# Kernel tuning notes

Hardware: AMD Instinct MI355X
Metric: run time of the kernel (lower is better)

## Reference

```python
import math
import jax, jax.numpy as jnp
import numpy as np

NUM_HEADS = 12
NUM_LANDMARKS = 32

def iterative_inv(mat, n_iter=6):
    # mat: [B, H, m, m] row-stochastic kernel; Newton-Schulz pseudo-inverse
    m = mat.shape[-1]
    I = jnp.eye(m, dtype=mat.dtype)
    K = mat
    # 'else' branch: per-(B,H) normalization by max column sum
    denom = jnp.max(jnp.sum(K, axis=-2), axis=-1)[..., None, None]
    V = jnp.swapaxes(K, -1, -2) / denom
    for _ in range(n_iter):
        KV = jnp.matmul(K, V)
        V = jnp.matmul(0.25 * V, 13.0 * I - jnp.matmul(KV, 15.0 * I - jnp.matmul(KV, 7.0 * I - KV)))
    return V

def setup_inputs() -> dict:
    key = jax.random.key(0)
    k1, k2, k3 = jax.random.split(key, 3)
    B, N, C = 8, 2048, 768
    x = jax.random.normal(k1, (B, N, C), dtype=jnp.float32)
    w_qkv = jax.random.normal(k2, (C, 3 * C), dtype=jnp.float32) * (1.0 / math.sqrt(C))
    w_proj = jax.random.normal(k3, (C, C), dtype=jnp.float32) * (1.0 / math.sqrt(C))
    b_proj = jnp.zeros((C,), dtype=jnp.float32)
    return {"x": x, "w_qkv": w_qkv, "w_proj": w_proj, "b_proj": b_proj}

def reference(x, w_qkv, w_proj, b_proj):
    B, N, C = x.shape
    H = NUM_HEADS
    d = C // H
    m = NUM_LANDMARKS
    qkv = (x @ w_qkv).reshape(B, N, 3, H, d).transpose(2, 0, 3, 1, 4)  # [3,B,H,N,d]
    Q, K, V = qkv[0], qkv[1], qkv[2]
    scale = 1.0 / math.sqrt(math.sqrt(d))
    Q = Q * scale
    K = K * scale
    # landmark pooling: mean over contiguous chunks of size N//m
    Q_l = Q.reshape(B, H, m, N // m, d).mean(axis=-2)  # [B,H,m,d]
    K_l = K.reshape(B, H, m, N // m, d).mean(axis=-2)
    kernel_1 = jax.nn.softmax(jnp.einsum('bhnd,bhmd->bhnm', Q, K_l), axis=-1)   # [B,H,N,m]
    kernel_2 = jax.nn.softmax(jnp.einsum('bhmd,bhkd->bhmk', Q_l, K_l), axis=-1) # [B,H,m,m]
    kernel_3 = jax.nn.softmax(jnp.einsum('bhmd,bhnd->bhmn', Q_l, K), axis=-1)   # [B,H,m,N]
    X = jnp.matmul(jnp.matmul(kernel_1, iterative_inv(kernel_2)), jnp.matmul(kernel_3, V))  # [B,H,N,d]
    X = X.transpose(0, 2, 1, 3).reshape(B, N, C)
    return X @ w_proj + b_proj
```

## Files before the change

### kernel.cpp

```cpp
#include <hip/hip_runtime.h>
#include <hip/hip_bf16.h>

typedef __hip_bfloat16 bf16;
typedef __attribute__((ext_vector_type(8))) __bf16 bf16x8;
typedef __attribute__((ext_vector_type(4))) float f32x4;

#define NB 8
#define SEQ 2048
#define CH 768
#define NH 12
#define HD 64
#define NL 32
#define BHT (NB*NH)
#define TOK (NB*SEQ)
#define QK_SCALE 0.35355339059327379f

#define BAR() __builtin_amdgcn_s_barrier()
#define WLGKM0() __asm__ __volatile__("s_waitcnt lgkmcnt(0)" ::: "memory")
#define WVM(n) __asm__ __volatile__("s_waitcnt vmcnt(" #n ")" ::: "memory")

__device__ __forceinline__ void async_ld16(const bf16* g, bf16* l) {
    unsigned loff = (unsigned)__builtin_amdgcn_readfirstlane((int)(unsigned)(uintptr_t)l);
    __builtin_amdgcn_global_load_lds(
        (const __attribute__((address_space(1))) unsigned*)(uintptr_t)g,
        (__attribute__((address_space(3))) unsigned*)(uintptr_t)loff, 16, 0, 0);
}

#define PREP_G0 (TOK*CH/2048)
#define PREP_G1 ((3*CH/32)*(CH/32))
#define PREP_G2 ((CH/32)*(CH/32))
__global__ __launch_bounds__(256) void prep(const float* __restrict__ x, bf16* __restrict__ xb,
                                            const float* __restrict__ w_qkv, bf16* __restrict__ wqkvT,
                                            const float* __restrict__ w_proj, bf16* __restrict__ wprojT) {
    __shared__ float tile[32][33];
    const int bid = blockIdx.x;
    const int t = threadIdx.x;
    if (bid < PREP_G0) {
        size_t i = ((size_t)bid * 256 + t) * 8;
        float4 a = *reinterpret_cast<const float4*>(x + i);
        float4 b = *reinterpret_cast<const float4*>(x + i + 4);
        alignas(16) bf16 tmp[8];
        tmp[0] = __float2bfloat16(a.x); tmp[1] = __float2bfloat16(a.y);
        tmp[2] = __float2bfloat16(a.z); tmp[3] = __float2bfloat16(a.w);
        tmp[4] = __float2bfloat16(b.x); tmp[5] = __float2bfloat16(b.y);
        tmp[6] = __float2bfloat16(b.z); tmp[7] = __float2bfloat16(b.w);
        *reinterpret_cast<uint4*>(xb + i) = *reinterpret_cast<const uint4*>(tmp);
        return;
    }
    const float* in; bf16* outp; int Hrows, Wcols, bx, by;
    if (bid < PREP_G0 + PREP_G1) {
        int tb = bid - PREP_G0;
        in = w_qkv; outp = wqkvT; Hrows = CH; Wcols = 3 * CH;
        bx = (tb % (3 * CH / 32)) * 32; by = (tb / (3 * CH / 32)) * 32;
    } else {
        int tb = bid - PREP_G0 - PREP_G1;
        in = w_proj; outp = wprojT; Hrows = CH; Wcols = CH;
        bx = (tb % (CH / 32)) * 32; by = (tb / (CH / 32)) * 32;
    }
    int tx = t & 31, ty = t >> 5;
    for (int i = 0; i < 32; i += 8)
        tile[ty + i][tx] = in[(size_t)(by + ty + i) * Wcols + bx + tx];
    __syncthreads();
    for (int i = 0; i < 32; i += 8)
        outp[(size_t)(bx + ty + i) * Hrows + by + tx] = __float2bfloat16(tile[tx][ty + i]);
}

template <int EPI>
__global__ __launch_bounds__(256, 2) void gemm_bt(
    const bf16* __restrict__ A, const bf16* __restrict__ Bt,
    int Nout, int Kdim,
    bf16* __restrict__ q, bf16* __restrict__ k, bf16* __restrict__ vt,
    float* __restrict__ Ql, float* __restrict__ Kl,
    float* __restrict__ outp, const float* __restrict__ bias_f) {
    __shared__ __align__(16) bf16 As[2][128 * 64];
    __shared__ __align__(16) bf16 Bs[2][192 * 64];
    const int t = threadIdx.x;
    const int wave = t >> 6, lane = t & 63;
    const int quad = lane >> 4, l15 = lane & 15;
    const int wr = wave >> 1, wc = wave & 1;

    int p = blockIdx.y * gridDim.x + blockIdx.x;
    int xcd = p & 7, j = p >> 3;
    int gx = gridDim.x;
    int bn = j % gx;
    int bm = (j / gx) * 8 + xcd;
    const int bm0 = bm * 128;
    const int bn0 = bn * 192;

    const int T = Kdim >> 6;

    const int srow = t >> 3;
    const int scol = (((t & 7) ^ (srow & 7)) << 3);
    const bf16* Abase = A + (size_t)(bm0 + srow) * Kdim + scol;
    const bf16* Bbase = Bt + (size_t)(bn0 + srow) * Kdim + scol;

    auto stA = [&](int kt, int c) {
        async_ld16(Abase + (size_t)(c * 32) * Kdim + kt * 64,
                   &As[kt & 1][c * 2048 + t * 8]);
    };
    auto stB = [&](int kt, int c) {
        async_ld16(Bbase + (size_t)(c * 32) * Kdim + kt * 64,
                   &Bs[kt & 1][c * 2048 + t * 8]);
    };

    const int swk[2] = { (quad ^ (l15 & 7)) << 3, ((4 + quad) ^ (l15 & 7)) << 3 };
    const bf16* arow = &As[0][(wr * 64 + l15) * 64];
    const bf16* brow = &Bs[0][(wc * 96 + l15) * 64];

    f32x4 acc[4][6];
    const f32x4 zero4 = {0.f, 0.f, 0.f, 0.f};
    #pragma unroll
    for (int i = 0; i < 4; i++)
        #pragma unroll
        for (int jj = 0; jj < 6; jj++) acc[i][jj] = zero4;

    stA(0, 0); stA(0, 2); stB(0, 0); stB(0, 1); stB(0, 3); stB(0, 4);
    stB(0, 2); stB(0, 5);
    stA(0, 1); stA(0, 3);
    WVM(4);
    BAR();

    bf16x8 a[4][2], b[6][2];
    for (int kt = 0; kt < T; kt++) {
        const int cur = kt & 1;
        const bool nxt = (kt + 1 < T);
        const bf16* ab = arow + cur * 8192;
        const bf16* bb = brow + cur * 12288;

        #pragma unroll
        for (int mi = 0; mi < 2; mi++)
            #pragma unroll
            for (int kk = 0; kk < 2; kk++)
                a[mi][kk] = *reinterpret_cast<const bf16x8*>(ab + mi * 1024 + swk[kk]);
        #pragma unroll
        for (int ni = 0; ni < 3; ni++)
            #pragma unroll
            for (int kk = 0; kk < 2; kk++)
                b[ni][kk] = *reinterpret_cast<const bf16x8*>(bb + ni * 1024 + swk[kk]);
        if (nxt) { stA(kt + 1, 0); stA(kt + 1, 2); stB(kt + 1, 0); }
        BAR(); WLGKM0();
        __builtin_amdgcn_s_setprio(1);
        #pragma unroll
        for (int mi = 0; mi < 2; mi++)
            #pragma unroll
            for (int ni = 0; ni < 3; ni++)
                #pragma unroll
                for (int kk = 0; kk < 2; kk++)
                    acc[mi][ni] = __builtin_amdgcn_mfma_f32_16x16x32_bf16(a[mi][kk], b[ni][kk], acc[mi][ni], 0, 0, 0);
        __builtin_amdgcn_s_setprio(0);
        if (nxt) { WVM(5); } else { WVM(2); }
        BAR();

        #pragma unroll
        for (int ni = 3; ni < 6; ni++)
            #pragma unroll
            for (int kk = 0; kk < 2; kk++)
                b[ni][kk] = *reinterpret_cast<const bf16x8*>(bb + ni * 1024 + swk[kk]);
        if (nxt) { stB(kt + 1, 1); stB(kt + 1, 3); stB(kt + 1, 4); }
        BAR(); WLGKM0();
        __builtin_amdgcn_s_setprio(1);
        #pragma unroll
        for (int mi = 0; mi < 2; mi++)
            #pragma unroll
            for (int ni = 3; ni < 6; ni++)
                #pragma unroll
                for (int kk = 0; kk < 2; kk++)
                    acc[mi][ni] = __builtin_amdgcn_mfma_f32_16x16x32_bf16(a[mi][kk], b[ni][kk], acc[mi][ni], 0, 0, 0);
        __builtin_amdgcn_s_setprio(0);
        if (nxt) { WVM(6); } else { WVM(0); }
        BAR();

        #pragma unroll
        for (int mi = 2; mi < 4; mi++)
            #pragma unroll
            for (int kk = 0; kk < 2; kk++)
                a[mi][kk] = *reinterpret_cast<const bf16x8*>(ab + mi * 1024 + swk[kk]);
        if (nxt) { stB(kt + 1, 2); stB(kt + 1, 5); stA(kt + 1, 1); stA(kt + 1, 3); }
        BAR(); WLGKM0();
        __builtin_amdgcn_s_setprio(1);
        #pragma unroll
        for (int mi = 2; mi < 4; mi++)
            #pragma unroll
            for (int ni = 0; ni < 6; ni++)
                #pragma unroll
                for (int kk = 0; kk < 2; kk++)
                    acc[mi][ni] = __builtin_amdgcn_mfma_f32_16x16x32_bf16(a[mi][kk], b[ni][kk], acc[mi][ni], 0, 0, 0);
        __builtin_amdgcn_s_setprio(0);
        if (nxt) { WVM(4); }
        BAR();
    }

    if (EPI == 0) {
        const int which = bn0 / CH;
        const int rem0 = bn0 - which * CH + wc * 96;
        const int b = bm0 >> 11;
        const int nnb = (bm0 & 2047) + wr * 64;
        if (which < 2) {
            bf16* dstqk = (which == 0) ? q : k;
            float* dstl = (which == 0) ? Ql : Kl;
            const int la = nnb >> 6;
            #pragma unroll
            for (int ni = 0; ni < 6; ni++) {
                int rem = rem0 + ni * 16;
                int h = rem >> 6;
                int dd = (rem & 63) + l15;
                int bh = b * NH + h;
                float colsum = 0.f;
                #pragma unroll
                for (int mi = 0; mi < 4; mi++) {
                    int nn0 = nnb + mi * 16 + quad * 4;
                    #pragma unroll
                    for (int r = 0; r < 4; r++) {
                        float val = acc[mi][ni][r];
                        colsum += val;
                        dstqk[((size_t)bh * SEQ + nn0 + r) * HD + dd] = __float2bfloat16(val * QK_SCALE);
                    }
                }
                colsum += __shfl_xor(colsum, 16);
                colsum += __shfl_xor(colsum, 32);
                if (quad == 0)
                    dstl[((size_t)bh * NL + la) * HD + dd] = colsum * (QK_SCALE / 64.f);
            }
        } else {
            #pragma unroll
            for (int ni = 0; ni < 6; ni++) {
                int rem = rem0 + ni * 16;
                int h = rem >> 6;
                int dd = (rem & 63) + l15;
                int bh = b * NH + h;
                #pragma unroll
                for (int mi = 0; mi < 4; mi++) {
                    int nn0 = nnb + mi * 16 + quad * 4;
                    alignas(8) bf16 four[4];
                    #pragma unroll
                    for (int r = 0; r < 4; r++) four[r] = __float2bfloat16(acc[mi][ni][r]);
                    *reinterpret_cast<uint2*>(&vt[((size_t)bh * HD + dd) * SEQ + nn0]) =
                        *reinterpret_cast<const uint2*>(four);
                }
            }
        }
    } else {
        #pragma unroll
        for (int ni = 0; ni < 6; ni++) {
            int col = bn0 + wc * 96 + ni * 16 + l15;
            float bb = bias_f[col];
            #pragma unroll
            for (int mi = 0; mi < 4; mi++)
                #pragma unroll
                for (int r = 0; r < 4; r++) {
                    int row = bm0 + wr * 64 + mi * 16 + quad * 4 + r;
                    outp[(size_t)row * Nout + col] = acc[mi][ni][r] + bb;
                }
        }
    }
}

__device__ inline void mm32(float* Cm, const float* Am, const float* Bm, int t) {
    for (int e = t; e < 1024; e += 256) {
        int i = e >> 5, jj = e & 31;
        float s = 0.f;
        #pragma unroll
        for (int kk = 0; kk < 32; kk++) s += Am[i * 32 + kk] * Bm[kk * 32 + jj];
        Cm[e] = s;
    }
}

__global__ __launch_bounds__(256) void k3_pv(const float* __restrict__ Ql,
                                             const float* __restrict__ Klm,
                                             const bf16* __restrict__ Kb,
                                             const bf16* __restrict__ Vt,
                                             float* __restrict__ Opart,
                                             float* __restrict__ Spart,
                                             float* __restrict__ Vinv) {
    __shared__ __align__(16) char smem[69632];
    const int bh = blockIdx.x;
    const int t = threadIdx.x;

    if (blockIdx.y == 0) {
        float* K2 = (float*)smem;
        float* Vv = K2 + 1024;
        float* KV = K2 + 2048;
        float* Ta = K2 + 3072;
        float* Tb = K2 + 4096;
        float* red = K2 + 5120;
        const float* ql = Ql + (size_t)bh * NL * HD;
        const float* kl = Klm + (size_t)bh * NL * HD;

        for (int e = t; e < 1024; e += 256) {
            int i = e >> 5, jj = e & 31;
            float s = 0.f;
            #pragma unroll 8
            for (int d = 0; d < 64; d++) s += ql[i * 64 + d] * kl[jj * 64 + d];
            K2[e] = s;
        }
        __syncthreads();
        if (t < 32) {
            float mx = -1e30f;
            for (int jj = 0; jj < 32; jj++) mx = fmaxf(mx, K2[t * 32 + jj]);
            float sm = 0.f;
            for (int jj = 0; jj < 32; jj++) { float e = __expf(K2[t * 32 + jj] - mx); K2[t * 32 + jj] = e; sm += e; }
            float inv = 1.f / sm;
            for (int jj = 0; jj < 32; jj++) K2[t * 32 + jj] *= inv;
        }
        __syncthreads();
        if (t < 32) {
            float cs = 0.f;
            for (int i = 0; i < 32; i++) cs += K2[i * 32 + t];
            red[t] = cs;
        }
        __syncthreads();
        if (t == 0) {
            float mx = red[0];
            for (int jj = 1; jj < 32; jj++) mx = fmaxf(mx, red[jj]);
            red[32] = mx;
        }
        __syncthreads();
        float invden = 1.f / red[32];
        for (int e = t; e < 1024; e += 256) {
            int i = e >> 5, jj = e & 31;
            Vv[e] = K2[jj * 32 + i] * invden;
        }
        __syncthreads();
        for (int it = 0; it < 6; it++) {
            mm32(KV, K2, Vv, t);
            __syncthreads();
            for (int e = t; e < 1024; e += 256) { int i = e >> 5, jj = e & 31; Ta[e] = ((i == jj) ? 7.f : 0.f) - KV[e]; }
            __syncthreads();
            mm32(Tb, KV, Ta, t);
            __syncthreads();
            for (int e = t; e < 1024; e += 256) { int i = e >> 5, jj = e & 31; Tb[e] = ((i == jj) ? 15.f : 0.f) - Tb[e]; }
            __syncthreads();
            mm32(Ta, KV, Tb, t);
            __syncthreads();
            for (int e = t; e < 1024; e += 256) { int i = e >> 5, jj = e & 31; Ta[e] = ((i == jj) ? 13.f : 0.f) - Ta[e]; }
            __syncthreads();
            mm32(Tb, Vv, Ta, t);
            __syncthreads();
            for (int e = t; e < 1024; e += 256) Vv[e] = 0.25f * Tb[e];
            __syncthreads();
        }
        for (int e = t; e < 1024; e += 256)
            Vinv[(size_t)bh * 1024 + e] = Vv[e];
        return;
    }

    bf16* Pw0 = (bf16*)smem;
    float* Ored0 = (float*)(smem + 34816);
    float* Sred = (float*)(smem + 34816 + 33280);
    const int cc = blockIdx.y - 1;
    const int n0 = cc * 512;
    const int w = t >> 6, lane = t & 63;
    const int quad = lane >> 4, l15 = lane & 15;

    const bf16* Kbh = Kb + (size_t)bh * SEQ * HD;
    const bf16* Vtb = Vt + (size_t)bh * HD * SEQ;

    bf16x8 af[2][2];
    #pragma unroll
    for (int mt = 0; mt < 2; mt++)
        #pragma unroll
        for (int kh = 0; kh < 2; kh++) {
            const float* src = Ql + (size_t)bh * NL * HD + (mt * 16 + l15) * 64 + kh * 32 + quad * 8;
            alignas(16) bf16 tmp[8];
            #pragma unroll
            for (int jj = 0; jj < 8; jj++) tmp[jj] = __float2bfloat16(src[jj]);
            af[mt][kh] = *reinterpret_cast<const bf16x8*>(tmp);
        }

    const f32x4 zero4 = {0.f, 0.f, 0.f, 0.f};
    f32x4 oacc[2][4];
    #pragma unroll
    for (int mt = 0; mt < 2; mt++)
        #pragma unroll
        for (int nd = 0; nd < 4; nd++) oacc[mt][nd] = zero4;
    float rs[2][4];
    #pragma unroll
    for (int mt = 0; mt < 2; mt++)
        #pragma unroll
        for (int r = 0; r < 4; r++) rs[mt][r] = 0.f;

    bf16* Pme = Pw0 + w * (32 * 136);

    #pragma unroll
    for (int h = 0; h < 2; h++) {
        f32x4 sacc[2][4];
        #pragma unroll
        for (int mt = 0; mt < 2; mt++)
            #pragma unroll
            for (int nt = 0; nt < 4; nt++) sacc[mt][nt] = zero4;
        #pragma unroll
        for (int nt = 0; nt < 4; nt++) {
            int n = n0 + w * 128 + h * 64 + nt * 16 + l15;
            bf16x8 kf0 = *reinterpret_cast<const bf16x8*>(&Kbh[(size_t)n * HD + quad * 8]);
            bf16x8 kf1 = *reinterpret_cast<const bf16x8*>(&Kbh[(size_t)n * HD + 32 + quad * 8]);
            #pragma unroll
            for (int mt = 0; mt < 2; mt++) {
                sacc[mt][nt] = __builtin_amdgcn_mfma_f32_16x16x32_bf16(af[mt][0], kf0, sacc[mt][nt], 0, 0, 0);
                sacc[mt][nt] = __builtin_amdgcn_mfma_f32_16x16x32_bf16(af[mt][1], kf1, sacc[mt][nt], 0, 0, 0);
            }
        }
        #pragma unroll
        for (int mt = 0; mt < 2; mt++)
            #pragma unroll
            for (int nt = 0; nt < 4; nt++)
                #pragma unroll
                for (int r = 0; r < 4; r++) {
                    float pv = __expf(sacc[mt][nt][r]);
                    rs[mt][r] += pv;
                    int row = mt * 16 + quad * 4 + r;
                    Pme[row * 136 + h * 64 + nt * 16 + l15] = __float2bfloat16(pv);
                }
    }
    __asm__ __volatile__("s_waitcnt lgkmcnt(0)" ::: "memory");

    #pragma unroll
    for (int kt = 0; kt < 4; kt++) {
        bf16x8 pa[2];
        pa[0] = *reinterpret_cast<const bf16x8*>(&Pme[l15 * 136 + kt * 32 + quad * 8]);
        pa[1] = *reinterpret_cast<const bf16x8*>(&Pme[(16 + l15) * 136 + kt * 32 + quad * 8]);
        int kbase = n0 + w * 128 + kt * 32 + quad * 8;
        #pragma unroll
        for (int nd = 0; nd < 4; nd++) {
            bf16x8 bv = *reinterpret_cast<const bf16x8*>(&Vtb[(size_t)(nd * 16 + l15) * SEQ + kbase]);
            oacc[0][nd] = __builtin_amdgcn_mfma_f32_16x16x32_bf16(pa[0], bv, oacc[0][nd], 0, 0, 0);
            oacc[1][nd] = __builtin_amdgcn_mfma_f32_16x16x32_bf16(pa[1], bv, oacc[1][nd], 0, 0, 0);
        }
    }

    #pragma unroll
    for (int mt = 0; mt < 2; mt++)
        #pragma unroll
        for (int r = 0; r < 4; r++) {
            float v = rs[mt][r];
            #pragma unroll
            for (int o = 1; o < 16; o <<= 1) v += __shfl_xor(v, o);
            rs[mt][r] = v;
        }
    if (l15 == 0)
        #pragma unroll
        for (int mt = 0; mt < 2; mt++)
            #pragma unroll
            for (int r = 0; r < 4; r++)
                Sred[w * 32 + mt * 16 + quad * 4 + r] = rs[mt][r];
    #pragma unroll
    for (int mt = 0; mt < 2; mt++)
        #pragma unroll
        for (int nd = 0; nd < 4; nd++)
            #pragma unroll
            for (int r = 0; r < 4; r++)
                Ored0[w * (32 * 65) + (mt * 16 + quad * 4 + r) * 65 + nd * 16 + l15] = oacc[mt][nd][r];
    __syncthreads();

    float* Op = Opart + ((size_t)bh * 4 + cc) * (NL * HD);
    for (int e = t; e < 2048; e += 256) {
        int m = e >> 6, dd = e & 63;
        Op[e] = Ored0[0 * (32 * 65) + m * 65 + dd] + Ored0[1 * (32 * 65) + m * 65 + dd] +
                Ored0[2 * (32 * 65) + m * 65 + dd] + Ored0[3 * (32 * 65) + m * 65 + dd];
    }
    if (t < 32)
        Spart[((size_t)bh * 4 + cc) * NL + t] = Sred[t] + Sred[32 + t] + Sred[64 + t] + Sred[96 + t];
}

__global__ __launch_bounds__(256) void combine_w2(const float* __restrict__ Opart,
                                                  const float* __restrict__ Spart,
                                                  const float* __restrict__ Vinv,
                                                  float* __restrict__ W2) {
    __shared__ float K3[2048];
    __shared__ float Vv[1024];
    __shared__ float stot[32];
    const int bh = blockIdx.x;
    const int t = threadIdx.x;

    if (t < 32) {
        const float* sp = Spart + (size_t)bh * 4 * NL;
        stot[t] = sp[t] + sp[32 + t] + sp[64 + t] + sp[96 + t];
    }
    {
        const float* op = Opart + (size_t)bh * 4 * (NL * HD);
        for (int e = t; e < 2048; e += 256)
            K3[e] = op[e] + op[2048 + e] + op[4096 + e] + op[6144 + e];
    }
    for (int e = t; e < 1024; e += 256)
        Vv[e] = Vinv[(size_t)bh * 1024 + e];
    __syncthreads();
    for (int e = t; e < 2048; e += 256) K3[e] *= (1.f / stot[e >> 6]);
    __syncthreads();
    for (int e = t; e < 2048; e += 256) {
        int i = e >> 6, dd = e & 63;
        float s = 0.f;
        #pragma unroll
        for (int kk = 0; kk < 32; kk++) s += Vv[i * 32 + kk] * K3[kk * 64 + dd];
        W2[(size_t)bh * NL * HD + e] = s;
    }
}

__global__ __launch_bounds__(256) void rows_fused(const bf16* __restrict__ Qb,
                                                  const float* __restrict__ Kl,
                                                  const float* __restrict__ W2,
                                                  bf16* __restrict__ Xp) {
    __shared__ __align__(16) bf16 Klb[32 * 64];
    __shared__ __align__(16) bf16 W2t[64 * 32];
    __shared__ __align__(16) bf16 Pw[4][32 * 40];
    const int bh = blockIdx.x, tile = blockIdx.y;
    const int t = threadIdx.x, w = t >> 6, lane = t & 63;
    const int quad = lane >> 4, l15 = lane & 15;

    {
        const float* ksrc = Kl + (size_t)bh * NL * HD;
        const float* wsrc = W2 + (size_t)bh * NL * HD;
        int e0 = t * 8;
        #pragma unroll
        for (int jj = 0; jj < 8; jj++) {
            int e = e0 + jj;
            Klb[e] = __float2bfloat16(ksrc[e]);
            int kk = e >> 6, dd = e & 63;
            W2t[dd * 32 + kk] = __float2bfloat16(wsrc[e]);
        }
    }
    __syncthreads();

    const int b = bh / NH, h = bh - b * NH;
    const int row0 = tile * 128 + w * 32;
    const bf16* qbase = Qb + ((size_t)bh * SEQ + row0) * HD;

    const f32x4 zero4 = {0.f, 0.f, 0.f, 0.f};
    f32x4 sacc[2][2];
    #pragma unroll
    for (int mt = 0; mt < 2; mt++)
        #pragma unroll
        for (int nt = 0; nt < 2; nt++) sacc[mt][nt] = zero4;
    #pragma unroll
    for (int kh = 0; kh < 2; kh++) {
        bf16x8 bk0 = *reinterpret_cast<const bf16x8*>(&Klb[(l15) * 64 + kh * 32 + quad * 8]);
        bf16x8 bk1 = *reinterpret_cast<const bf16x8*>(&Klb[(16 + l15) * 64 + kh * 32 + quad * 8]);
        #pragma unroll
        for (int mt = 0; mt < 2; mt++) {
            bf16x8 aq = *reinterpret_cast<const bf16x8*>(&qbase[(size_t)(mt * 16 + l15) * HD + kh * 32 + quad * 8]);
            sacc[mt][0] = __builtin_amdgcn_mfma_f32_16x16x32_bf16(aq, bk0, sacc[mt][0], 0, 0, 0);
            sacc[mt][1] = __builtin_amdgcn_mfma_f32_16x16x32_bf16(aq, bk1, sacc[mt][1], 0, 0, 0);
        }
    }

    float invs[2][4];
    bf16* Pme = &Pw[w][0];
    #pragma unroll
    for (int mt = 0; mt < 2; mt++)
        #pragma unroll
        for (int r = 0; r < 4; r++) {
            float v0 = __expf(sacc[mt][0][r]);
            float v1 = __expf(sacc[mt][1][r]);
            int row = mt * 16 + quad * 4 + r;
            Pme[row * 40 + l15] = __float2bfloat16(v0);
            Pme[row * 40 + 16 + l15] = __float2bfloat16(v1);
            float v = v0 + v1;
            #pragma unroll
            for (int o = 1; o < 16; o <<= 1) v += __shfl_xor(v, o);
            invs[mt][r] = 1.f / v;
        }
    __asm__ __volatile__("s_waitcnt lgkmcnt(0)" ::: "memory");

    f32x4 oacc[2][4];
    #pragma unroll
    for (int mt = 0; mt < 2; mt++)
        #pragma unroll
        for (int nd = 0; nd < 4; nd++) oacc[mt][nd] = zero4;
    bf16x8 pa[2];
    pa[0] = *reinterpret_cast<const bf16x8*>(&Pme[l15 * 40 + quad * 8]);
    pa[1] = *reinterpret_cast<const bf16x8*>(&Pme[(16 + l15) * 40 + quad * 8]);
    #pragma unroll
    for (int nd = 0; nd < 4; nd++) {
        bf16x8 bw = *reinterpret_cast<const bf16x8*>(&W2t[(nd * 16 + l15) * 32 + quad * 8]);
        oacc[0][nd] = __builtin_amdgcn_mfma_f32_16x16x32_bf16(pa[0], bw, oacc[0][nd], 0, 0, 0);
        oacc[1][nd] = __builtin_amdgcn_mfma_f32_16x16x32_bf16(pa[1], bw, oacc[1][nd], 0, 0, 0);
    }

    #pragma unroll
    for (int mt = 0; mt < 2; mt++)
        #pragma unroll
        for (int nd = 0; nd < 4; nd++)
            #pragma unroll
            for (int r = 0; r < 4; r++) {
                int row = row0 + mt * 16 + quad * 4 + r;
                Xp[((size_t)(b * SEQ + row)) * CH + h * 64 + nd * 16 + l15] =
                    __float2bfloat16(oacc[mt][nd][r] * invs[mt][r]);
            }
}

extern "C" void kernel_launch(void* const* d_in, const int* in_sizes, int n_in,
                              void* d_out, int out_size, void* d_ws, size_t ws_size,
                              hipStream_t stream) {
    const float* x      = (const float*)d_in[0];
    const float* w_qkv  = (const float*)d_in[1];
    const float* w_proj = (const float*)d_in[2];
    const float* b_proj = (const float*)d_in[3];
    float* out = (float*)d_out;

    char* ws = (char*)d_ws;
    size_t off = 0;
    auto alloc = [&](size_t bytes) -> void* {
        void* p = ws + off;
        off += (bytes + 255) & ~(size_t)255;
        return p;
    };
    bf16* wqkvT  = (bf16*)alloc((size_t)3 * CH * CH * 2);
    bf16* wprojT = (bf16*)alloc((size_t)CH * CH * 2);
    bf16* Qb     = (bf16*)alloc((size_t)BHT * SEQ * HD * 2);
    bf16* Kb     = (bf16*)alloc((size_t)BHT * SEQ * HD * 2);
    bf16* Vt     = (bf16*)alloc((size_t)BHT * SEQ * HD * 2);
    float* Ql    = (float*)alloc((size_t)BHT * NL * HD * 4);
    float* Kl    = (float*)alloc((size_t)BHT * NL * HD * 4);
    float* Opart = (float*)alloc((size_t)BHT * 4 * NL * HD * 4);
    float* Spart = (float*)alloc((size_t)BHT * 4 * NL * 4);
    float* Vinv  = (float*)alloc((size_t)BHT * NL * NL * 4);
    float* W2    = (float*)alloc((size_t)BHT * NL * HD * 4);
    bf16* Xp     = (bf16*)alloc((size_t)TOK * CH * 2);
    if (ws_size < off) return;
    bf16* xb = Xp;

    prep<<<PREP_G0 + PREP_G1 + PREP_G2, 256, 0, stream>>>(x, xb, w_qkv, wqkvT, w_proj, wprojT);

    gemm_bt<0><<<dim3((3 * CH) / 192, TOK / 128), 256, 0, stream>>>(
        xb, wqkvT, 3 * CH, CH, Qb, Kb, Vt, Ql, Kl, nullptr, nullptr);

    k3_pv<<<dim3(BHT, 5), 256, 0, stream>>>(Ql, Kl, Kb, Vt, Opart, Spart, Vinv);
    combine_w2<<<BHT, 256, 0, stream>>>(Opart, Spart, Vinv, W2);
    rows_fused<<<dim3(BHT, SEQ / 128), 256, 0, stream>>>(Qb, Kl, W2, Xp);

    gemm_bt<1><<<dim3(CH / 192, TOK / 128), 256, 0, stream>>>(
        Xp, wprojT, CH, CH, nullptr, nullptr, nullptr, nullptr, nullptr, out, b_proj);
}
```

Before: 263.5 us.

## Use 512-thread GEMM blocks with eight waves and a single-barrier pipeline

The bf16 GEMM kernel moves from 4 waves (each computing a 64x96 sub-tile) to 8 waves in a 2x4 grid (each computing 64x48), launched with 512 threads. The three-phase interleaved load/compute schedule with several barriers per k-step is replaced by a simpler one: all next-tile async loads are issued at the top, then the whole sub-tile is computed, then one wait and one barrier. The goal is more waves to hide latency and less per-wave register pressure. In exchange it loses the fine-grained overlap of loads with MFMA work. The new launch bound of 4 blocks of 512 threads may also cap registers tightly enough to cause spills, and the 80 KB of LDS per block limits how many blocks can actually co-reside.

```diff
diff --git a/kernel.cpp b/kernel.cpp
--- a/kernel.cpp
+++ b/kernel.cpp
@@ -16,7 +16,6 @@
 #define QK_SCALE 0.35355339059327379f
 
 #define BAR() __builtin_amdgcn_s_barrier()
-#define WLGKM0() __asm__ __volatile__("s_waitcnt lgkmcnt(0)" ::: "memory")
 #define WVM(n) __asm__ __volatile__("s_waitcnt vmcnt(" #n ")" ::: "memory")
 
 __device__ __forceinline__ void async_ld16(const bf16* g, bf16* l) {
@@ -66,7 +65,7 @@
 }
 
 template <int EPI>
-__global__ __launch_bounds__(256, 2) void gemm_bt(
+__global__ __launch_bounds__(512, 4) void gemm_bt(
     const bf16* __restrict__ A, const bf16* __restrict__ Bt,
     int Nout, int Kdim,
     bf16* __restrict__ q, bf16* __restrict__ k, bf16* __restrict__ vt,
@@ -77,7 +76,7 @@
     const int t = threadIdx.x;
     const int wave = t >> 6, lane = t & 63;
     const int quad = lane >> 4, l15 = lane & 15;
-    const int wr = wave >> 1, wc = wave & 1;
+    const int wr = wave >> 2, wc = wave & 3;
 
     int p = blockIdx.y * gridDim.x + blockIdx.x;
     int xcd = p & 7, j = p >> 3;
@@ -95,40 +94,39 @@
     const bf16* Bbase = Bt + (size_t)(bn0 + srow) * Kdim + scol;
 
     auto stA = [&](int kt, int c) {
-        async_ld16(Abase + (size_t)(c * 32) * Kdim + kt * 64,
-                   &As[kt & 1][c * 2048 + t * 8]);
+        async_ld16(Abase + (size_t)(c * 64) * Kdim + kt * 64,
+                   &As[kt & 1][c * 4096 + t * 8]);
     };
     auto stB = [&](int kt, int c) {
-        async_ld16(Bbase + (size_t)(c * 32) * Kdim + kt * 64,
-                   &Bs[kt & 1][c * 2048 + t * 8]);
+        async_ld16(Bbase + (size_t)(c * 64) * Kdim + kt * 64,
+                   &Bs[kt & 1][c * 4096 + t * 8]);
     };
 
     const int swk[2] = { (quad ^ (l15 & 7)) << 3, ((4 + quad) ^ (l15 & 7)) << 3 };
     const bf16* arow = &As[0][(wr * 64 + l15) * 64];
-    const bf16* brow = &Bs[0][(wc * 96 + l15) * 64];
-
-    f32x4 acc[4][6];
+    const bf16* brow = &Bs[0][(wc * 48 + l15) * 64];
+
+    f32x4 acc[4][3];
     const f32x4 zero4 = {0.f, 0.f, 0.f, 0.f};
     #pragma unroll
     for (int i = 0; i < 4; i++)
         #pragma unroll
-        for (int jj = 0; jj < 6; jj++) acc[i][jj] = zero4;
-
-    stA(0, 0); stA(0, 2); stB(0, 0); stB(0, 1); stB(0, 3); stB(0, 4);
-    stB(0, 2); stB(0, 5);
-    stA(0, 1); stA(0, 3);
-    WVM(4);
+        for (int jj = 0; jj < 3; jj++) acc[i][jj] = zero4;
+
+    stA(0, 0); stA(0, 1); stB(0, 0); stB(0, 1); stB(0, 2);
+    WVM(0);
     BAR();
 
-    bf16x8 a[4][2], b[6][2];
     for (int kt = 0; kt < T; kt++) {
-        const int cur = kt & 1;
         const bool nxt = (kt + 1 < T);
-        const bf16* ab = arow + cur * 8192;
-        const bf16* bb = brow + cur * 12288;
-
-        #pragma unroll
-        for (int mi = 0; mi < 2; mi++)
+        const bf16* ab = arow + (kt & 1) * 8192;
+        const bf16* bb = brow + (kt & 1) * 12288;
+
+        if (nxt) { stA(kt + 1, 0); stA(kt + 1, 1); stB(kt + 1, 0); stB(kt + 1, 1); stB(kt + 1, 2); }
+
+        bf16x8 a[4][2], b[3][2];
+        #pragma unroll
+        for (int mi = 0; mi < 4; mi++)
             #pragma unroll
             for (int kk = 0; kk < 2; kk++)
                 a[mi][kk] = *reinterpret_cast<const bf16x8*>(ab + mi * 1024 + swk[kk]);
@@ -137,62 +135,23 @@
             #pragma unroll
             for (int kk = 0; kk < 2; kk++)
                 b[ni][kk] = *reinterpret_cast<const bf16x8*>(bb + ni * 1024 + swk[kk]);
-        if (nxt) { stA(kt + 1, 0); stA(kt + 1, 2); stB(kt + 1, 0); }
-        BAR(); WLGKM0();
+
         __builtin_amdgcn_s_setprio(1);
         #pragma unroll
-        for (int mi = 0; mi < 2; mi++)
+        for (int mi = 0; mi < 4; mi++)
             #pragma unroll
             for (int ni = 0; ni < 3; ni++)
                 #pragma unroll
                 for (int kk = 0; kk < 2; kk++)
                     acc[mi][ni] = __builtin_amdgcn_mfma_f32_16x16x32_bf16(a[mi][kk], b[ni][kk], acc[mi][ni], 0, 0, 0);
         __builtin_amdgcn_s_setprio(0);
-        if (nxt) { WVM(5); } else { WVM(2); }
-        BAR();
-
-        #pragma unroll
-        for (int ni = 3; ni < 6; ni++)
-            #pragma unroll
-            for (int kk = 0; kk < 2; kk++)
-                b[ni][kk] = *reinterpret_cast<const bf16x8*>(bb + ni * 1024 + swk[kk]);
-        if (nxt) { stB(kt + 1, 1); stB(kt + 1, 3); stB(kt + 1, 4); }
-        BAR(); WLGKM0();
-        __builtin_amdgcn_s_setprio(1);
-        #pragma unroll
-        for (int mi = 0; mi < 2; mi++)
-            #pragma unroll
-            for (int ni = 3; ni < 6; ni++)
-                #pragma unroll
-                for (int kk = 0; kk < 2; kk++)
-                    acc[mi][ni] = __builtin_amdgcn_mfma_f32_16x16x32_bf16(a[mi][kk], b[ni][kk], acc[mi][ni], 0, 0, 0);
-        __builtin_amdgcn_s_setprio(0);
-        if (nxt) { WVM(6); } else { WVM(0); }
-        BAR();
-
-        #pragma unroll
-        for (int mi = 2; mi < 4; mi++)
-            #pragma unroll
-            for (int kk = 0; kk < 2; kk++)
-                a[mi][kk] = *reinterpret_cast<const bf16x8*>(ab + mi * 1024 + swk[kk]);
-        if (nxt) { stB(kt + 1, 2); stB(kt + 1, 5); stA(kt + 1, 1); stA(kt + 1, 3); }
-        BAR(); WLGKM0();
-        __builtin_amdgcn_s_setprio(1);
-        #pragma unroll
-        for (int mi = 2; mi < 4; mi++)
-            #pragma unroll
-            for (int ni = 0; ni < 6; ni++)
-                #pragma unroll
-                for (int kk = 0; kk < 2; kk++)
-                    acc[mi][ni] = __builtin_amdgcn_mfma_f32_16x16x32_bf16(a[mi][kk], b[ni][kk], acc[mi][ni], 0, 0, 0);
-        __builtin_amdgcn_s_setprio(0);
-        if (nxt) { WVM(4); }
-        BAR();
+
+        if (nxt) { WVM(0); BAR(); }
     }
 
     if (EPI == 0) {
         const int which = bn0 / CH;
-        const int rem0 = bn0 - which * CH + wc * 96;
+        const int rem0 = bn0 - which * CH + wc * 48;
         const int b = bm0 >> 11;
         const int nnb = (bm0 & 2047) + wr * 64;
         if (which < 2) {
@@ -200,7 +159,7 @@
             float* dstl = (which == 0) ? Ql : Kl;
             const int la = nnb >> 6;
             #pragma unroll
-            for (int ni = 0; ni < 6; ni++) {
+            for (int ni = 0; ni < 3; ni++) {
                 int rem = rem0 + ni * 16;
                 int h = rem >> 6;
                 int dd = (rem & 63) + l15;
@@ -223,7 +182,7 @@
             }
         } else {
             #pragma unroll
-            for (int ni = 0; ni < 6; ni++) {
+            for (int ni = 0; ni < 3; ni++) {
                 int rem = rem0 + ni * 16;
                 int h = rem >> 6;
                 int dd = (rem & 63) + l15;
@@ -241,8 +200,8 @@
         }
     } else {
         #pragma unroll
-        for (int ni = 0; ni < 6; ni++) {
-            int col = bn0 + wc * 96 + ni * 16 + l15;
+        for (int ni = 0; ni < 3; ni++) {
+            int col = bn0 + wc * 48 + ni * 16 + l15;
             float bb = bias_f[col];
             #pragma unroll
             for (int mi = 0; mi < 4; mi++)
@@ -619,13 +578,13 @@
 
     prep<<<PREP_G0 + PREP_G1 + PREP_G2, 256, 0, stream>>>(x, xb, w_qkv, wqkvT, w_proj, wprojT);
 
-    gemm_bt<0><<<dim3((3 * CH) / 192, TOK / 128), 256, 0, stream>>>(
+    gemm_bt<0><<<dim3((3 * CH) / 192, TOK / 128), 512, 0, stream>>>(
         xb, wqkvT, 3 * CH, CH, Qb, Kb, Vt, Ql, Kl, nullptr, nullptr);
 
     k3_pv<<<dim3(BHT, 5), 256, 0, stream>>>(Ql, Kl, Kb, Vt, Opart, Spart, Vinv);
     combine_w2<<<BHT, 256, 0, stream>>>(Opart, Spart, Vinv, W2);
     rows_fused<<<dim3(BHT, SEQ / 128), 256, 0, stream>>>(Qb, Kl, W2, Xp);
 
-    gemm_bt<1><<<dim3(CH / 192, TOK / 128), 256, 0, stream>>>(
+    gemm_bt<1><<<dim3(CH / 192, TOK / 128), 512, 0, stream>>>(
         Xp, wprojT, CH, CH, nullptr, nullptr, nullptr, nullptr, nullptr, out, b_proj);
 }
```

Result: no change. 259.0 us (-1.7%).
